# Performance work log

Measured on AMD Instinct MI355X. Metric: run time of the kernel, lower is better.

## Reference

```python
import jax, jax.numpy as jnp
import numpy as np
from jax import lax

H = 512   # hidden_size
O = 256   # output_size
B = 64    # batch
S = 1024  # encoder sequence length
T = 256   # decoder timesteps


def setup_inputs() -> dict:
    key = jax.random.key(0)
    ks = jax.random.split(key, 10)
    bound = 1.0 / np.sqrt(H)  # PyTorch LSTM/Linear init scale
    return {
        "encoder_outputs": jax.random.normal(ks[0], (B, S, H), jnp.float32),
        "hidden": jax.random.normal(ks[1], (1, B, H), jnp.float32),
        "cell": jax.random.normal(ks[2], (1, B, H), jnp.float32),
        "target": jax.random.normal(ks[3], (B, T, O), jnp.float32),
        # LSTM params (gate order i, f, g, o as in PyTorch)
        "W_ih": jax.random.uniform(ks[4], (4 * H, H + O), jnp.float32, -bound, bound),
        "W_hh": jax.random.uniform(ks[5], (4 * H, H), jnp.float32, -bound, bound),
        "b_ih": jax.random.uniform(ks[6], (4 * H,), jnp.float32, -bound, bound),
        "b_hh": jax.random.uniform(ks[7], (4 * H,), jnp.float32, -bound, bound),
        # FC params
        "W_fc": jax.random.uniform(ks[8], (O, H), jnp.float32, -bound, bound),
        "b_fc": jax.random.uniform(ks[9], (O,), jnp.float32, -bound, bound),
    }


def reference(encoder_outputs, hidden, cell, target, W_ih, W_hh, b_ih, b_hh, W_fc, b_fc):
    h0 = hidden[0]  # [B, H]
    c0 = cell[0]    # [B, H]

    def step(carry, x_t):
        h, c = carry
        # Attention: dot-product scores over encoder positions
        scores = jnp.einsum("bsh,bh->bs", encoder_outputs, h)      # [B, S]
        attn = jax.nn.softmax(scores, axis=1)
        context = jnp.einsum("bs,bsh->bh", attn, encoder_outputs)  # [B, H]
        x = jnp.concatenate([context, x_t], axis=-1)               # [B, H+O]
        # Single-step LSTM cell (PyTorch gate order i, f, g, o)
        gates = x @ W_ih.T + b_ih + h @ W_hh.T + b_hh              # [B, 4H]
        i_g, f_g, g_g, o_g = jnp.split(gates, 4, axis=-1)
        i_g = jax.nn.sigmoid(i_g)
        f_g = jax.nn.sigmoid(f_g)
        g_g = jnp.tanh(g_g)
        o_g = jax.nn.sigmoid(o_g)
        c_new = f_g * c + i_g * g_g
        h_new = o_g * jnp.tanh(c_new)
        out = h_new @ W_fc.T + b_fc                                # [B, O]
        return (h_new, c_new), out

    _, outs = lax.scan(step, (h0, c0), jnp.swapaxes(target, 0, 1))  # outs: [T, B, O]
    return jnp.swapaxes(outs, 0, 1)  # [B, T, O]
```

## Files before the change

### kernel.cpp

```cpp
#include <hip/hip_runtime.h>

#define HH 512
#define OO 256
#define BB 64
#define SS 1024
#define TT 256
#define KK 1280

typedef __attribute__((ext_vector_type(8))) short bh8;
typedef __attribute__((ext_vector_type(8))) _Float16 hf8;
typedef __attribute__((ext_vector_type(4))) float fx4;

__device__ __forceinline__ unsigned short f2bf(float x) {
    union { float f; unsigned int u; } v; v.f = x;
    unsigned int r = v.u + 0x7fffu + ((v.u >> 16) & 1u);
    return (unsigned short)(r >> 16);
}
__device__ __forceinline__ float bf2f(unsigned short s) {
    union { unsigned int u; float f; } z; z.u = ((unsigned int)s) << 16; return z.f;
}

__global__ void prep_weights(const float* __restrict__ W_ih,
                             const float* __restrict__ W_hh,
                             unsigned short* __restrict__ wfH,
                             unsigned short* __restrict__ wfL) {
    int g = blockIdx.x * 256 + threadIdx.x;
    if (g >= 64 * 40 * 2 * 64) return;
    int lane = g & 63;
    int nt = (g >> 6) & 1;
    int kk = (g >> 7) % 40;
    int ht = (g >> 7) / 40;
    int c = nt * 16 + (lane & 15);
    int gate = c >> 3, rr = c & 7;
    int j = gate * 512 + ht * 8 + rr;
    int kbase = kk * 32 + (lane >> 4) * 8;
    unsigned short* dh = wfH + (size_t)g * 8;
    unsigned short* dl = wfL + (size_t)g * 8;
#pragma unroll
    for (int r = 0; r < 8; ++r) {
        int k = kbase + r;
        float v = (k < 768) ? W_ih[(size_t)j * 768 + k]
                            : W_hh[(size_t)j * 512 + (k - 768)];
        unsigned short hi = f2bf(v);
        dh[r] = hi;
        dl[r] = f2bf(v - bf2f(hi));
    }
}

__global__ void prep_misc(const float* __restrict__ hidden,
                          const float* __restrict__ cell,
                          float* __restrict__ h, float* __restrict__ c) {
    const int total = 32768 + 32768;
    for (int i = blockIdx.x * 256 + threadIdx.x; i < total; i += gridDim.x * 256) {
        if (i < 32768) h[i] = hidden[i];
        else           c[i - 32768] = cell[i - 32768];
    }
}

__global__ void prep_enc(const float* __restrict__ enc,
                         _Float16* __restrict__ ench) {
    const size_t i = ((size_t)blockIdx.x * 256 + threadIdx.x) * 8;
    const float4 a = *(const float4*)(enc + i);
    const float4 b = *(const float4*)(enc + i + 4);
    hf8 o;
    o[0] = (_Float16)a.x; o[1] = (_Float16)a.y;
    o[2] = (_Float16)a.z; o[3] = (_Float16)a.w;
    o[4] = (_Float16)b.x; o[5] = (_Float16)b.y;
    o[6] = (_Float16)b.z; o[7] = (_Float16)b.w;
    *(hf8*)(ench + i) = o;
}

__device__ __forceinline__ void fc_unit(int v, int tprev,
                                        const float* __restrict__ h,
                                        const float* __restrict__ W_fc,
                                        const float* __restrict__ b_fc,
                                        float* __restrict__ out,
                                        float (*shacc)[64]) {
    const int tid = threadIdx.x;
    const int b = v >> 2, oq = v & 3;
    const int ol = tid & 63, kq = tid >> 6;
    const int o = oq * 64 + ol;
    float acc = 0.f;
    const float* hp = h + b * HH + kq * 128;
    const float* wp = W_fc + (size_t)o * HH + kq * 128;
#pragma unroll 8
    for (int k2 = 0; k2 < 128; ++k2) acc += hp[k2] * wp[k2];
    shacc[kq][ol] = acc;
    __syncthreads();
    if (tid < 64) {
        float vv = shacc[0][tid] + shacc[1][tid]
                 + shacc[2][tid] + shacc[3][tid] + b_fc[oq * 64 + tid];
        out[((size_t)b * TT + tprev) * OO + oq * 64 + tid] = vv;
    }
}

template <int ENCF16>
__global__ void __launch_bounds__(256)
step_attnp(int t, const float* __restrict__ enc,
           const _Float16* __restrict__ ench,
           const float* __restrict__ h,
           float* __restrict__ pm, float* __restrict__ pl,
           float* __restrict__ pctx,
           const float* __restrict__ W_fc, const float* __restrict__ b_fc,
           float* __restrict__ out) {
    const int tid = threadIdx.x;
    const int lane = tid & 63;
    const int w = tid >> 6;

    __shared__ union {
        struct { float m[4]; float l[4]; float ctx[4][512]; } a;
        struct { float acc[4][64]; } o;
    } sh;

    const int u = blockIdx.x;
    if (u < 1024) {
        const int b = u >> 4, ch = u & 15;
        float m = -3.0e38f, l = 0.f;
        if (ENCF16) {
            const float* hb = h + b * HH + lane * 8;
            const float4 h0 = *(const float4*)hb;
            const float4 h1 = *(const float4*)(hb + 4);
            float cx[8];
#pragma unroll
            for (int j = 0; j < 8; ++j) cx[j] = 0.f;
            const _Float16* er =
                ench + ((size_t)(b * SS + ch * 64 + w * 16)) * HH + lane * 8;
            for (int rp = 0; rp < 8; ++rp) {
                const hf8 ev = *(const hf8*)er;
                const hf8 fv = *(const hf8*)(er + HH);
                float e[8], f[8];
#pragma unroll
                for (int j = 0; j < 8; ++j) {
                    e[j] = (float)ev[j];
                    f[j] = (float)fv[j];
                }
                float dA = e[0]*h0.x + e[1]*h0.y + e[2]*h0.z + e[3]*h0.w
                         + e[4]*h1.x + e[5]*h1.y + e[6]*h1.z + e[7]*h1.w;
                float dB = f[0]*h0.x + f[1]*h0.y + f[2]*h0.z + f[3]*h0.w
                         + f[4]*h1.x + f[5]*h1.y + f[6]*h1.z + f[7]*h1.w;
#pragma unroll
                for (int off = 32; off; off >>= 1) {
                    dA += __shfl_xor(dA, off);
                    dB += __shfl_xor(dB, off);
                }
                const float mx = fmaxf(dA, dB);
                if (mx > m) {
                    const float fs = __expf(m - mx);
                    l *= fs;
#pragma unroll
                    for (int j = 0; j < 8; ++j) cx[j] *= fs;
                    m = mx;
                }
                const float pA = __expf(dA - m);
                const float pB = __expf(dB - m);
                l += pA + pB;
#pragma unroll
                for (int j = 0; j < 8; ++j) cx[j] += pA * e[j] + pB * f[j];
                er += 2 * HH;
            }
            if (lane == 0) { sh.a.m[w] = m; sh.a.l[w] = l; }
            *(float4*)&sh.a.ctx[w][lane * 8]     = make_float4(cx[0], cx[1], cx[2], cx[3]);
            *(float4*)&sh.a.ctx[w][lane * 8 + 4] = make_float4(cx[4], cx[5], cx[6], cx[7]);
        } else {
            const float4 h0 = *(const float4*)(h + b * HH + lane * 4);
            const float4 h1 = *(const float4*)(h + b * HH + 256 + lane * 4);
            float4 c0 = {0, 0, 0, 0}, c1 = {0, 0, 0, 0};
            const float* er = enc + ((size_t)(b * SS + ch * 64 + w * 16)) * HH;
            for (int rp = 0; rp < 8; ++rp) {
                const float4 e0 = *(const float4*)(er + lane * 4);
                const float4 e1 = *(const float4*)(er + 256 + lane * 4);
                const float4 f0 = *(const float4*)(er + HH + lane * 4);
                const float4 f1 = *(const float4*)(er + HH + 256 + lane * 4);
                float dA = e0.x * h0.x + e0.y * h0.y + e0.z * h0.z + e0.w * h0.w
                         + e1.x * h1.x + e1.y * h1.y + e1.z * h1.z + e1.w * h1.w;
                float dB = f0.x * h0.x + f0.y * h0.y + f0.z * h0.z + f0.w * h0.w
                         + f1.x * h1.x + f1.y * h1.y + f1.z * h1.z + f1.w * h1.w;
#pragma unroll
                for (int off = 32; off; off >>= 1) {
                    dA += __shfl_xor(dA, off);
                    dB += __shfl_xor(dB, off);
                }
                const float mx = fmaxf(dA, dB);
                if (mx > m) {
                    const float fs = __expf(m - mx);
                    l *= fs;
                    c0.x *= fs; c0.y *= fs; c0.z *= fs; c0.w *= fs;
                    c1.x *= fs; c1.y *= fs; c1.z *= fs; c1.w *= fs;
                    m = mx;
                }
                const float pA = __expf(dA - m);
                const float pB = __expf(dB - m);
                l += pA + pB;
                c0.x += pA * e0.x + pB * f0.x; c0.y += pA * e0.y + pB * f0.y;
                c0.z += pA * e0.z + pB * f0.z; c0.w += pA * e0.w + pB * f0.w;
                c1.x += pA * e1.x + pB * f1.x; c1.y += pA * e1.y + pB * f1.y;
                c1.z += pA * e1.z + pB * f1.z; c1.w += pA * e1.w + pB * f1.w;
                er += 2 * HH;
            }
            if (lane == 0) { sh.a.m[w] = m; sh.a.l[w] = l; }
            *(float4*)&sh.a.ctx[w][lane * 4] = c0;
            *(float4*)&sh.a.ctx[w][256 + lane * 4] = c1;
        }
        __syncthreads();
        float M = fmaxf(fmaxf(sh.a.m[0], sh.a.m[1]), fmaxf(sh.a.m[2], sh.a.m[3]));
        float wg[4]; float ls = 0.f;
#pragma unroll
        for (int q = 0; q < 4; ++q) { wg[q] = __expf(sh.a.m[q] - M); ls += wg[q] * sh.a.l[q]; }
        const int hh = tid * 2;
        float v0 = wg[0] * sh.a.ctx[0][hh] + wg[1] * sh.a.ctx[1][hh]
                 + wg[2] * sh.a.ctx[2][hh] + wg[3] * sh.a.ctx[3][hh];
        float v1 = wg[0] * sh.a.ctx[0][hh + 1] + wg[1] * sh.a.ctx[1][hh + 1]
                 + wg[2] * sh.a.ctx[2][hh + 1] + wg[3] * sh.a.ctx[3][hh + 1];
        float* pc = pctx + ((size_t)(b * 16 + ch)) * HH;
        *(float2*)(pc + hh) = make_float2(v0, v1);
        if (tid == 0) { pm[b * 16 + ch] = M; pl[b * 16 + ch] = ls; }
    } else if (t > 0) {
        fc_unit(u - 1024, t - 1, h, W_fc, b_fc, out, sh.o.acc);
    }
}

__global__ void __launch_bounds__(256)
step_combine(int t, const float* __restrict__ target, const float* __restrict__ h,
             const float* __restrict__ pm, const float* __restrict__ pl,
             const float* __restrict__ pctx,
             unsigned short* __restrict__ xbh, unsigned short* __restrict__ xbl) {
    const int tid = threadIdx.x;
    const int b = blockIdx.x;
    float Mb = -3.0e38f;
#pragma unroll
    for (int q2 = 0; q2 < 16; ++q2) Mb = fmaxf(Mb, pm[b * 16 + q2]);
    float wq[16]; float lsb = 0.f;
#pragma unroll
    for (int q2 = 0; q2 < 16; ++q2) {
        wq[q2] = __expf(pm[b * 16 + q2] - Mb);
        lsb += wq[q2] * pl[b * 16 + q2];
    }
    const float inv = 1.0f / lsb;
    const int h2 = tid * 2;
    float s0 = 0.f, s1 = 0.f;
#pragma unroll
    for (int q2 = 0; q2 < 16; ++q2) {
        const float* pc2 = pctx + ((size_t)(b * 16 + q2)) * HH + h2;
        s0 += wq[q2] * pc2[0];
        s1 += wq[q2] * pc2[1];
    }
    s0 *= inv; s1 *= inv;
    unsigned short a0 = f2bf(s0), a1 = f2bf(s1);
    xbh[b * KK + h2]     = a0;  xbl[b * KK + h2]     = f2bf(s0 - bf2f(a0));
    xbh[b * KK + h2 + 1] = a1;  xbl[b * KK + h2 + 1] = f2bf(s1 - bf2f(a1));
    if (tid < 128) {
        const float* tg = target + ((size_t)b * TT + t) * OO + tid * 2;
        unsigned short t0 = f2bf(tg[0]), t1 = f2bf(tg[1]);
        xbh[b * KK + 512 + tid * 2]     = t0;
        xbh[b * KK + 512 + tid * 2 + 1] = t1;
        xbl[b * KK + 512 + tid * 2]     = f2bf(tg[0] - bf2f(t0));
        xbl[b * KK + 512 + tid * 2 + 1] = f2bf(tg[1] - bf2f(t1));
    }
    const float hv0 = h[b * HH + h2], hv1 = h[b * HH + h2 + 1];
    unsigned short g0 = f2bf(hv0), g1 = f2bf(hv1);
    xbh[b * KK + 768 + h2]     = g0;  xbl[b * KK + 768 + h2]     = f2bf(hv0 - bf2f(g0));
    xbh[b * KK + 768 + h2 + 1] = g1;  xbl[b * KK + 768 + h2 + 1] = f2bf(hv1 - bf2f(g1));
}

__global__ void __launch_bounds__(256)
step_gates(const unsigned short* __restrict__ xbh,
           const unsigned short* __restrict__ xbl,
           const unsigned short* __restrict__ wfH,
           const unsigned short* __restrict__ wfL,
           const float* __restrict__ b_ih, const float* __restrict__ b_hh,
           float* __restrict__ h, float* __restrict__ c) {
    const int tid = threadIdx.x;
    const int lane = tid & 63;
    const int w = tid >> 6;
    __shared__ float g[64][32];

    const int ht = blockIdx.x;
    fx4 a0 = {0, 0, 0, 0}, a1 = {0, 0, 0, 0};
    const int bro = 16 * w + (lane & 15);
    const int kg = lane >> 4;
    const size_t wbase = (size_t)ht * 40 * 2 * 512;
    for (int kk = 0; kk < 40; ++kk) {
        const size_t aoff = (size_t)bro * KK + kk * 32 + kg * 8;
        bh8 avh = *(const bh8*)(xbh + aoff);
        bh8 avl = *(const bh8*)(xbl + aoff);
        bh8 b0h = *(const bh8*)(wfH + wbase + (kk * 2 + 0) * 512 + lane * 8);
        bh8 b1h = *(const bh8*)(wfH + wbase + (kk * 2 + 1) * 512 + lane * 8);
        bh8 b0l = *(const bh8*)(wfL + wbase + (kk * 2 + 0) * 512 + lane * 8);
        bh8 b1l = *(const bh8*)(wfL + wbase + (kk * 2 + 1) * 512 + lane * 8);
        a0 = __builtin_amdgcn_mfma_f32_16x16x32_bf16(avh, b0h, a0, 0, 0, 0);
        a0 = __builtin_amdgcn_mfma_f32_16x16x32_bf16(avl, b0h, a0, 0, 0, 0);
        a0 = __builtin_amdgcn_mfma_f32_16x16x32_bf16(avh, b0l, a0, 0, 0, 0);
        a1 = __builtin_amdgcn_mfma_f32_16x16x32_bf16(avh, b1h, a1, 0, 0, 0);
        a1 = __builtin_amdgcn_mfma_f32_16x16x32_bf16(avl, b1h, a1, 0, 0, 0);
        a1 = __builtin_amdgcn_mfma_f32_16x16x32_bf16(avh, b1l, a1, 0, 0, 0);
    }
    const int crow = (lane >> 4) * 4;
#pragma unroll
    for (int r = 0; r < 4; ++r) {
        g[16 * w + crow + r][lane & 15]        = a0[r];
        g[16 * w + crow + r][16 + (lane & 15)] = a1[r];
    }
    __syncthreads();
#pragma unroll
    for (int p = 0; p < 2; ++p) {
        const int idx = tid * 2 + p;
        const int b = idx >> 3, r = idx & 7;
        const int hidx = ht * 8 + r;
        float gi = g[b][r]      + b_ih[hidx]        + b_hh[hidx];
        float gf = g[b][8 + r]  + b_ih[512 + hidx]  + b_hh[512 + hidx];
        float gg = g[b][16 + r] + b_ih[1024 + hidx] + b_hh[1024 + hidx];
        float go = g[b][24 + r] + b_ih[1536 + hidx] + b_hh[1536 + hidx];
        float ig = 1.f / (1.f + __expf(-gi));
        float fg = 1.f / (1.f + __expf(-gf));
        float g2 = tanhf(gg);
        float og = 1.f / (1.f + __expf(-go));
        float cn = fg * c[b * HH + hidx] + ig * g2;
        float hn = og * tanhf(cn);
        c[b * HH + hidx] = cn;
        h[b * HH + hidx] = hn;
    }
}

__global__ void __launch_bounds__(256)
fc_final(const float* __restrict__ h, const float* __restrict__ W_fc,
         const float* __restrict__ b_fc, float* __restrict__ out) {
    __shared__ float acc[4][64];
    fc_unit(blockIdx.x, TT - 1, h, W_fc, b_fc, out, acc);
}

extern "C" void kernel_launch(void* const* d_in, const int* in_sizes, int n_in,
                              void* d_out, int out_size, void* d_ws, size_t ws_size,
                              hipStream_t stream) {
    const float* enc    = (const float*)d_in[0];
    const float* hidden = (const float*)d_in[1];
    const float* cellp  = (const float*)d_in[2];
    const float* target = (const float*)d_in[3];
    const float* W_ih   = (const float*)d_in[4];
    const float* W_hh   = (const float*)d_in[5];
    const float* b_ih   = (const float*)d_in[6];
    const float* b_hh   = (const float*)d_in[7];
    const float* W_fc   = (const float*)d_in[8];
    const float* b_fc   = (const float*)d_in[9];
    float* out = (float*)d_out;

    char* base = (char*)d_ws;
    float* h              = (float*)(base + 0);
    float* c              = (float*)(base + 131072);
    unsigned short* wfH   = (unsigned short*)(base + 262144);
    unsigned short* wfL   = (unsigned short*)(base + 5505024);
    unsigned short* xbh   = (unsigned short*)(base + 10747904);
    unsigned short* xbl   = (unsigned short*)(base + 10911744);
    float* pm             = (float*)(base + 11075584);
    float* pl             = (float*)(base + 11079680);
    float* pctx           = (float*)(base + 11083776);
    _Float16* ench        = (_Float16*)(base + 13180928);
    const size_t NEED_H = 13180928ULL + 67108864ULL;

    const bool use_ench = (ws_size >= NEED_H);

    prep_weights<<<dim3(1280), dim3(256), 0, stream>>>(W_ih, W_hh, wfH, wfL);
    prep_misc<<<dim3(256), dim3(256), 0, stream>>>(hidden, cellp, h, c);
    if (use_ench)
        prep_enc<<<dim3(16384), dim3(256), 0, stream>>>(enc, ench);

    for (int t = 0; t < TT; ++t) {
        if (use_ench)
            step_attnp<1><<<dim3(1280), dim3(256), 0, stream>>>(
                t, enc, ench, h, pm, pl, pctx, W_fc, b_fc, out);
        else
            step_attnp<0><<<dim3(1280), dim3(256), 0, stream>>>(
                t, enc, ench, h, pm, pl, pctx, W_fc, b_fc, out);
        step_combine<<<dim3(64), dim3(256), 0, stream>>>(
            t, target, h, pm, pl, pctx, xbh, xbl);
        step_gates<<<dim3(64), dim3(256), 0, stream>>>(
            xbh, xbl, wfH, wfL, b_ih, b_hh, h, c);
    }
    fc_final<<<dim3(256), dim3(256), 0, stream>>>(h, W_fc, b_fc, out);
}
```

Before: 10.53 ms.

## Fuse attention partial and combine into one per-batch 1024-thread kernel

Attention now runs one 1024-thread block per batch row (16 waves each covering 64 encoder rows) instead of 16 blocks per batch row. The softmax/context merge and the bf16 hi/lo packing of the LSTM input now happen inside the same kernel, so the separate combine launch and the global partial buffers go away. The FC blocks are also reshaped to one 1024-thread block per batch. This saves a launch and global round-trip per timestep, but drops parallelism from 1280 blocks to 128, which may underuse the GPU's compute units on the bandwidth-heavy attention pass. The fp32 encoder fallback path is removed, so the kernel now always assumes the fp16 workspace is present.

```diff
diff --git a/kernel.cpp b/kernel.cpp
--- a/kernel.cpp
+++ b/kernel.cpp
@@ -70,37 +70,10 @@
     *(hf8*)(ench + i) = o;
 }
 
-__device__ __forceinline__ void fc_unit(int v, int tprev,
-                                        const float* __restrict__ h,
-                                        const float* __restrict__ W_fc,
-                                        const float* __restrict__ b_fc,
-                                        float* __restrict__ out,
-                                        float (*shacc)[64]) {
-    const int tid = threadIdx.x;
-    const int b = v >> 2, oq = v & 3;
-    const int ol = tid & 63, kq = tid >> 6;
-    const int o = oq * 64 + ol;
-    float acc = 0.f;
-    const float* hp = h + b * HH + kq * 128;
-    const float* wp = W_fc + (size_t)o * HH + kq * 128;
-#pragma unroll 8
-    for (int k2 = 0; k2 < 128; ++k2) acc += hp[k2] * wp[k2];
-    shacc[kq][ol] = acc;
-    __syncthreads();
-    if (tid < 64) {
-        float vv = shacc[0][tid] + shacc[1][tid]
-                 + shacc[2][tid] + shacc[3][tid] + b_fc[oq * 64 + tid];
-        out[((size_t)b * TT + tprev) * OO + oq * 64 + tid] = vv;
-    }
-}
-
-template <int ENCF16>
-__global__ void __launch_bounds__(256)
-step_attnp(int t, const float* __restrict__ enc,
-           const _Float16* __restrict__ ench,
-           const float* __restrict__ h,
-           float* __restrict__ pm, float* __restrict__ pl,
-           float* __restrict__ pctx,
+__global__ void __launch_bounds__(1024)
+step_attnx(int t, const _Float16* __restrict__ ench,
+           const float* __restrict__ h, const float* __restrict__ target,
+           unsigned short* __restrict__ xbh, unsigned short* __restrict__ xbl,
            const float* __restrict__ W_fc, const float* __restrict__ b_fc,
            float* __restrict__ out) {
     const int tid = threadIdx.x;
@@ -108,158 +81,107 @@
     const int w = tid >> 6;
 
     __shared__ union {
-        struct { float m[4]; float l[4]; float ctx[4][512]; } a;
-        struct { float acc[4][64]; } o;
+        struct { float m[16]; float l[16]; float ctx[16][512]; } a;
+        struct { float acc[256][4]; } o;
     } sh;
 
-    const int u = blockIdx.x;
-    if (u < 1024) {
-        const int b = u >> 4, ch = u & 15;
+    const int bid = blockIdx.x;
+    if (bid < 64) {
+        const int b = bid;
+        const float* hb = h + b * HH + lane * 8;
+        const float4 h0 = *(const float4*)hb;
+        const float4 h1 = *(const float4*)(hb + 4);
         float m = -3.0e38f, l = 0.f;
-        if (ENCF16) {
-            const float* hb = h + b * HH + lane * 8;
-            const float4 h0 = *(const float4*)hb;
-            const float4 h1 = *(const float4*)(hb + 4);
-            float cx[8];
-#pragma unroll
-            for (int j = 0; j < 8; ++j) cx[j] = 0.f;
-            const _Float16* er =
-                ench + ((size_t)(b * SS + ch * 64 + w * 16)) * HH + lane * 8;
-            for (int rp = 0; rp < 8; ++rp) {
-                const hf8 ev = *(const hf8*)er;
-                const hf8 fv = *(const hf8*)(er + HH);
-                float e[8], f[8];
-#pragma unroll
-                for (int j = 0; j < 8; ++j) {
-                    e[j] = (float)ev[j];
-                    f[j] = (float)fv[j];
-                }
-                float dA = e[0]*h0.x + e[1]*h0.y + e[2]*h0.z + e[3]*h0.w
-                         + e[4]*h1.x + e[5]*h1.y + e[6]*h1.z + e[7]*h1.w;
-                float dB = f[0]*h0.x + f[1]*h0.y + f[2]*h0.z + f[3]*h0.w
-                         + f[4]*h1.x + f[5]*h1.y + f[6]*h1.z + f[7]*h1.w;
-#pragma unroll
-                for (int off = 32; off; off >>= 1) {
-                    dA += __shfl_xor(dA, off);
-                    dB += __shfl_xor(dB, off);
-                }
-                const float mx = fmaxf(dA, dB);
-                if (mx > m) {
-                    const float fs = __expf(m - mx);
-                    l *= fs;
-#pragma unroll
-                    for (int j = 0; j < 8; ++j) cx[j] *= fs;
-                    m = mx;
-                }
-                const float pA = __expf(dA - m);
-                const float pB = __expf(dB - m);
-                l += pA + pB;
-#pragma unroll
-                for (int j = 0; j < 8; ++j) cx[j] += pA * e[j] + pB * f[j];
-                er += 2 * HH;
+        float cx[8];
+#pragma unroll
+        for (int j = 0; j < 8; ++j) cx[j] = 0.f;
+        const _Float16* er = ench + ((size_t)(b * SS + w * 64)) * HH + lane * 8;
+        for (int rp = 0; rp < 32; ++rp) {
+            const hf8 ev = *(const hf8*)er;
+            const hf8 fv = *(const hf8*)(er + HH);
+            float e[8], f[8];
+#pragma unroll
+            for (int j = 0; j < 8; ++j) {
+                e[j] = (float)ev[j];
+                f[j] = (float)fv[j];
             }
-            if (lane == 0) { sh.a.m[w] = m; sh.a.l[w] = l; }
-            *(float4*)&sh.a.ctx[w][lane * 8]     = make_float4(cx[0], cx[1], cx[2], cx[3]);
-            *(float4*)&sh.a.ctx[w][lane * 8 + 4] = make_float4(cx[4], cx[5], cx[6], cx[7]);
+            float dA = e[0]*h0.x + e[1]*h0.y + e[2]*h0.z + e[3]*h0.w
+                     + e[4]*h1.x + e[5]*h1.y + e[6]*h1.z + e[7]*h1.w;
+            float dB = f[0]*h0.x + f[1]*h0.y + f[2]*h0.z + f[3]*h0.w
+                     + f[4]*h1.x + f[5]*h1.y + f[6]*h1.z + f[7]*h1.w;
+#pragma unroll
+            for (int off = 32; off; off >>= 1) {
+                dA += __shfl_xor(dA, off);
+                dB += __shfl_xor(dB, off);
+            }
+            const float mx = fmaxf(dA, dB);
+            if (mx > m) {
+                const float fs = __expf(m - mx);
+                l *= fs;
+#pragma unroll
+                for (int j = 0; j < 8; ++j) cx[j] *= fs;
+                m = mx;
+            }
+            const float pA = __expf(dA - m);
+            const float pB = __expf(dB - m);
+            l += pA + pB;
+#pragma unroll
+            for (int j = 0; j < 8; ++j) cx[j] += pA * e[j] + pB * f[j];
+            er += 2 * HH;
+        }
+        if (lane == 0) { sh.a.m[w] = m; sh.a.l[w] = l; }
+        *(float4*)&sh.a.ctx[w][lane * 8]     = make_float4(cx[0], cx[1], cx[2], cx[3]);
+        *(float4*)&sh.a.ctx[w][lane * 8 + 4] = make_float4(cx[4], cx[5], cx[6], cx[7]);
+        __syncthreads();
+        float M = -3.0e38f;
+#pragma unroll
+        for (int q = 0; q < 16; ++q) M = fmaxf(M, sh.a.m[q]);
+        float wq[16]; float lsb = 0.f;
+#pragma unroll
+        for (int q = 0; q < 16; ++q) {
+            wq[q] = __expf(sh.a.m[q] - M);
+            lsb += wq[q] * sh.a.l[q];
+        }
+        const float inv = 1.0f / lsb;
+        if (tid < 512) {
+            float s = 0.f;
+#pragma unroll
+            for (int q = 0; q < 16; ++q) s += wq[q] * sh.a.ctx[q][tid];
+            s *= inv;
+            const unsigned short a0 = f2bf(s);
+            xbh[b * KK + tid] = a0;
+            xbl[b * KK + tid] = f2bf(s - bf2f(a0));
+        } else if (tid < 768) {
+            const int o = tid - 512;
+            const float tv = target[((size_t)b * TT + t) * OO + o];
+            const unsigned short t0 = f2bf(tv);
+            xbh[b * KK + 512 + o] = t0;
+            xbl[b * KK + 512 + o] = f2bf(tv - bf2f(t0));
         } else {
-            const float4 h0 = *(const float4*)(h + b * HH + lane * 4);
-            const float4 h1 = *(const float4*)(h + b * HH + 256 + lane * 4);
-            float4 c0 = {0, 0, 0, 0}, c1 = {0, 0, 0, 0};
-            const float* er = enc + ((size_t)(b * SS + ch * 64 + w * 16)) * HH;
-            for (int rp = 0; rp < 8; ++rp) {
-                const float4 e0 = *(const float4*)(er + lane * 4);
-                const float4 e1 = *(const float4*)(er + 256 + lane * 4);
-                const float4 f0 = *(const float4*)(er + HH + lane * 4);
-                const float4 f1 = *(const float4*)(er + HH + 256 + lane * 4);
-                float dA = e0.x * h0.x + e0.y * h0.y + e0.z * h0.z + e0.w * h0.w
-                         + e1.x * h1.x + e1.y * h1.y + e1.z * h1.z + e1.w * h1.w;
-                float dB = f0.x * h0.x + f0.y * h0.y + f0.z * h0.z + f0.w * h0.w
-                         + f1.x * h1.x + f1.y * h1.y + f1.z * h1.z + f1.w * h1.w;
-#pragma unroll
-                for (int off = 32; off; off >>= 1) {
-                    dA += __shfl_xor(dA, off);
-                    dB += __shfl_xor(dB, off);
-                }
-                const float mx = fmaxf(dA, dB);
-                if (mx > m) {
-                    const float fs = __expf(m - mx);
-                    l *= fs;
-                    c0.x *= fs; c0.y *= fs; c0.z *= fs; c0.w *= fs;
-                    c1.x *= fs; c1.y *= fs; c1.z *= fs; c1.w *= fs;
-                    m = mx;
-                }
-                const float pA = __expf(dA - m);
-                const float pB = __expf(dB - m);
-                l += pA + pB;
-                c0.x += pA * e0.x + pB * f0.x; c0.y += pA * e0.y + pB * f0.y;
-                c0.z += pA * e0.z + pB * f0.z; c0.w += pA * e0.w + pB * f0.w;
-                c1.x += pA * e1.x + pB * f1.x; c1.y += pA * e1.y + pB * f1.y;
-                c1.z += pA * e1.z + pB * f1.z; c1.w += pA * e1.w + pB * f1.w;
-                er += 2 * HH;
-            }
-            if (lane == 0) { sh.a.m[w] = m; sh.a.l[w] = l; }
-            *(float4*)&sh.a.ctx[w][lane * 4] = c0;
-            *(float4*)&sh.a.ctx[w][256 + lane * 4] = c1;
+            const int h2 = (tid - 768) * 2;
+            const float hv0 = h[b * HH + h2], hv1 = h[b * HH + h2 + 1];
+            const unsigned short g0 = f2bf(hv0), g1 = f2bf(hv1);
+            xbh[b * KK + 768 + h2]     = g0;
+            xbl[b * KK + 768 + h2]     = f2bf(hv0 - bf2f(g0));
+            xbh[b * KK + 768 + h2 + 1] = g1;
+            xbl[b * KK + 768 + h2 + 1] = f2bf(hv1 - bf2f(g1));
         }
+    } else if (t > 0) {
+        const int b = bid - 64;
+        const int o = tid & 255, kq = tid >> 8;
+        float acc = 0.f;
+        const float* hp = h + b * HH + kq * 128;
+        const float* wp = W_fc + (size_t)o * HH + kq * 128;
+#pragma unroll 8
+        for (int k2 = 0; k2 < 128; ++k2) acc += hp[k2] * wp[k2];
+        sh.o.acc[o][kq] = acc;
         __syncthreads();
-        float M = fmaxf(fmaxf(sh.a.m[0], sh.a.m[1]), fmaxf(sh.a.m[2], sh.a.m[3]));
-        float wg[4]; float ls = 0.f;
-#pragma unroll
-        for (int q = 0; q < 4; ++q) { wg[q] = __expf(sh.a.m[q] - M); ls += wg[q] * sh.a.l[q]; }
-        const int hh = tid * 2;
-        float v0 = wg[0] * sh.a.ctx[0][hh] + wg[1] * sh.a.ctx[1][hh]
-                 + wg[2] * sh.a.ctx[2][hh] + wg[3] * sh.a.ctx[3][hh];
-        float v1 = wg[0] * sh.a.ctx[0][hh + 1] + wg[1] * sh.a.ctx[1][hh + 1]
-                 + wg[2] * sh.a.ctx[2][hh + 1] + wg[3] * sh.a.ctx[3][hh + 1];
-        float* pc = pctx + ((size_t)(b * 16 + ch)) * HH;
-        *(float2*)(pc + hh) = make_float2(v0, v1);
-        if (tid == 0) { pm[b * 16 + ch] = M; pl[b * 16 + ch] = ls; }
-    } else if (t > 0) {
-        fc_unit(u - 1024, t - 1, h, W_fc, b_fc, out, sh.o.acc);
-    }
-}
-
-__global__ void __launch_bounds__(256)
-step_combine(int t, const float* __restrict__ target, const float* __restrict__ h,
-             const float* __restrict__ pm, const float* __restrict__ pl,
-             const float* __restrict__ pctx,
-             unsigned short* __restrict__ xbh, unsigned short* __restrict__ xbl) {
-    const int tid = threadIdx.x;
-    const int b = blockIdx.x;
-    float Mb = -3.0e38f;
-#pragma unroll
-    for (int q2 = 0; q2 < 16; ++q2) Mb = fmaxf(Mb, pm[b * 16 + q2]);
-    float wq[16]; float lsb = 0.f;
-#pragma unroll
-    for (int q2 = 0; q2 < 16; ++q2) {
-        wq[q2] = __expf(pm[b * 16 + q2] - Mb);
-        lsb += wq[q2] * pl[b * 16 + q2];
-    }
-    const float inv = 1.0f / lsb;
-    const int h2 = tid * 2;
-    float s0 = 0.f, s1 = 0.f;
-#pragma unroll
-    for (int q2 = 0; q2 < 16; ++q2) {
-        const float* pc2 = pctx + ((size_t)(b * 16 + q2)) * HH + h2;
-        s0 += wq[q2] * pc2[0];
-        s1 += wq[q2] * pc2[1];
-    }
-    s0 *= inv; s1 *= inv;
-    unsigned short a0 = f2bf(s0), a1 = f2bf(s1);
-    xbh[b * KK + h2]     = a0;  xbl[b * KK + h2]     = f2bf(s0 - bf2f(a0));
-    xbh[b * KK + h2 + 1] = a1;  xbl[b * KK + h2 + 1] = f2bf(s1 - bf2f(a1));
-    if (tid < 128) {
-        const float* tg = target + ((size_t)b * TT + t) * OO + tid * 2;
-        unsigned short t0 = f2bf(tg[0]), t1 = f2bf(tg[1]);
-        xbh[b * KK + 512 + tid * 2]     = t0;
-        xbh[b * KK + 512 + tid * 2 + 1] = t1;
-        xbl[b * KK + 512 + tid * 2]     = f2bf(tg[0] - bf2f(t0));
-        xbl[b * KK + 512 + tid * 2 + 1] = f2bf(tg[1] - bf2f(t1));
-    }
-    const float hv0 = h[b * HH + h2], hv1 = h[b * HH + h2 + 1];
-    unsigned short g0 = f2bf(hv0), g1 = f2bf(hv1);
-    xbh[b * KK + 768 + h2]     = g0;  xbl[b * KK + 768 + h2]     = f2bf(hv0 - bf2f(g0));
-    xbh[b * KK + 768 + h2 + 1] = g1;  xbl[b * KK + 768 + h2 + 1] = f2bf(hv1 - bf2f(g1));
+        if (tid < 256) {
+            float vv = sh.o.acc[tid][0] + sh.o.acc[tid][1]
+                     + sh.o.acc[tid][2] + sh.o.acc[tid][3] + b_fc[tid];
+            out[((size_t)b * TT + (t - 1)) * OO + tid] = vv;
+        }
+    }
 }
 
 __global__ void __launch_bounds__(256)
@@ -321,11 +243,24 @@
     }
 }
 
-__global__ void __launch_bounds__(256)
+__global__ void __launch_bounds__(1024)
 fc_final(const float* __restrict__ h, const float* __restrict__ W_fc,
          const float* __restrict__ b_fc, float* __restrict__ out) {
-    __shared__ float acc[4][64];
-    fc_unit(blockIdx.x, TT - 1, h, W_fc, b_fc, out, acc);
+    __shared__ float acc[256][4];
+    const int tid = threadIdx.x;
+    const int b = blockIdx.x;
+    const int o = tid & 255, kq = tid >> 8;
+    float a = 0.f;
+    const float* hp = h + b * HH + kq * 128;
+    const float* wp = W_fc + (size_t)o * HH + kq * 128;
+#pragma unroll 8
+    for (int k2 = 0; k2 < 128; ++k2) a += hp[k2] * wp[k2];
+    acc[o][kq] = a;
+    __syncthreads();
+    if (tid < 256) {
+        float vv = acc[tid][0] + acc[tid][1] + acc[tid][2] + acc[tid][3] + b_fc[tid];
+        out[((size_t)b * TT + (TT - 1)) * OO + tid] = vv;
+    }
 }
 
 extern "C" void kernel_launch(void* const* d_in, const int* in_sizes, int n_in,
@@ -350,30 +285,17 @@
     unsigned short* wfL   = (unsigned short*)(base + 5505024);
     unsigned short* xbh   = (unsigned short*)(base + 10747904);
     unsigned short* xbl   = (unsigned short*)(base + 10911744);
-    float* pm             = (float*)(base + 11075584);
-    float* pl             = (float*)(base + 11079680);
-    float* pctx           = (float*)(base + 11083776);
-    _Float16* ench        = (_Float16*)(base + 13180928);
-    const size_t NEED_H = 13180928ULL + 67108864ULL;
-
-    const bool use_ench = (ws_size >= NEED_H);
+    _Float16* ench        = (_Float16*)(base + 11075584);
 
     prep_weights<<<dim3(1280), dim3(256), 0, stream>>>(W_ih, W_hh, wfH, wfL);
     prep_misc<<<dim3(256), dim3(256), 0, stream>>>(hidden, cellp, h, c);
-    if (use_ench)
-        prep_enc<<<dim3(16384), dim3(256), 0, stream>>>(enc, ench);
+    prep_enc<<<dim3(16384), dim3(256), 0, stream>>>(enc, ench);
 
     for (int t = 0; t < TT; ++t) {
-        if (use_ench)
-            step_attnp<1><<<dim3(1280), dim3(256), 0, stream>>>(
-                t, enc, ench, h, pm, pl, pctx, W_fc, b_fc, out);
-        else
-            step_attnp<0><<<dim3(1280), dim3(256), 0, stream>>>(
-                t, enc, ench, h, pm, pl, pctx, W_fc, b_fc, out);
-        step_combine<<<dim3(64), dim3(256), 0, stream>>>(
-            t, target, h, pm, pl, pctx, xbh, xbl);
+        step_attnx<<<dim3(128), dim3(1024), 0, stream>>>(
+            t, ench, h, target, xbh, xbl, W_fc, b_fc, out);
         step_gates<<<dim3(64), dim3(256), 0, stream>>>(
             xbh, xbl, wfH, wfL, b_ih, b_hh, h, c);
     }
-    fc_final<<<dim3(256), dim3(256), 0, stream>>>(h, W_fc, b_fc, out);
-}
+    fc_final<<<dim3(64), dim3(1024), 0, stream>>>(h, W_fc, b_fc, out);
+}
```

Result: slower. 13.33 ms (+26.6%).

## Compute attention scores with f16 MFMA on a pre-swizzled encoder copy

Applied to the files above, without the earlier changes.

Adds a prep kernel that lays out fp16 encoder data in MFMA fragment order, so attention scores can come from 16x16x32 f16 MFMA against an fp16 copy of h held in shared memory. The per-row shuffle reductions and the online softmax are replaced by a block-wide max/sum followed by a second pass that accumulates the context from a row-major fp16 (or fp32) encoder copy. This moves the score dot products off scalar FMAs, but each step now reads the encoder twice and the workspace needs a second 64MB copy. Rounding h to fp16 may also reduce accuracy.

```diff
diff --git a/kernel.cpp b/kernel.cpp
--- a/kernel.cpp
+++ b/kernel.cpp
@@ -10,20 +10,21 @@
 typedef __attribute__((ext_vector_type(8))) short bh8;
 typedef __attribute__((ext_vector_type(8))) _Float16 hf8;
 typedef __attribute__((ext_vector_type(4))) float fx4;
-
-__device__ __forceinline__ unsigned short f2bf(float x) {
+typedef unsigned short ushort_t;
+
+__device__ __forceinline__ ushort_t f2bf(float x) {
     union { float f; unsigned int u; } v; v.f = x;
     unsigned int r = v.u + 0x7fffu + ((v.u >> 16) & 1u);
-    return (unsigned short)(r >> 16);
-}
-__device__ __forceinline__ float bf2f(unsigned short s) {
+    return (ushort_t)(r >> 16);
+}
+__device__ __forceinline__ float bf2f(ushort_t s) {
     union { unsigned int u; float f; } z; z.u = ((unsigned int)s) << 16; return z.f;
 }
 
 __global__ void prep_weights(const float* __restrict__ W_ih,
                              const float* __restrict__ W_hh,
-                             unsigned short* __restrict__ wfH,
-                             unsigned short* __restrict__ wfL) {
+                             ushort_t* __restrict__ wfH,
+                             ushort_t* __restrict__ wfL) {
     int g = blockIdx.x * 256 + threadIdx.x;
     if (g >= 64 * 40 * 2 * 64) return;
     int lane = g & 63;
@@ -34,14 +35,14 @@
     int gate = c >> 3, rr = c & 7;
     int j = gate * 512 + ht * 8 + rr;
     int kbase = kk * 32 + (lane >> 4) * 8;
-    unsigned short* dh = wfH + (size_t)g * 8;
-    unsigned short* dl = wfL + (size_t)g * 8;
+    ushort_t* dh = wfH + (size_t)g * 8;
+    ushort_t* dl = wfL + (size_t)g * 8;
 #pragma unroll
     for (int r = 0; r < 8; ++r) {
         int k = kbase + r;
         float v = (k < 768) ? W_ih[(size_t)j * 768 + k]
                             : W_hh[(size_t)j * 512 + (k - 768)];
-        unsigned short hi = f2bf(v);
+        ushort_t hi = f2bf(v);
         dh[r] = hi;
         dl[r] = f2bf(v - bf2f(hi));
     }
@@ -57,8 +58,29 @@
     }
 }
 
-__global__ void prep_enc(const float* __restrict__ enc,
-                         _Float16* __restrict__ ench) {
+__global__ void prep_encfrag(const float* __restrict__ enc,
+                             _Float16* __restrict__ encfrag) {
+    const int g = blockIdx.x * 256 + threadIdx.x;
+    const int lane = g & 63;
+    const int kk = (g >> 6) & 15;
+    const int w = (g >> 10) & 3;
+    const int ch = (g >> 12) & 15;
+    const int b = g >> 16;
+    const int s = ch * 64 + w * 16 + (lane & 15);
+    const int k0 = kk * 32 + (lane >> 4) * 8;
+    const float* src = enc + ((size_t)(b * SS + s)) * HH + k0;
+    const float4 a = *(const float4*)src;
+    const float4 bb = *(const float4*)(src + 4);
+    hf8 o;
+    o[0] = (_Float16)a.x;  o[1] = (_Float16)a.y;
+    o[2] = (_Float16)a.z;  o[3] = (_Float16)a.w;
+    o[4] = (_Float16)bb.x; o[5] = (_Float16)bb.y;
+    o[6] = (_Float16)bb.z; o[7] = (_Float16)bb.w;
+    *(hf8*)(encfrag + (size_t)g * 8) = o;
+}
+
+__global__ void prep_ench(const float* __restrict__ enc,
+                          _Float16* __restrict__ ench) {
     const size_t i = ((size_t)blockIdx.x * 256 + threadIdx.x) * 8;
     const float4 a = *(const float4*)(enc + i);
     const float4 b = *(const float4*)(enc + i + 4);
@@ -94,10 +116,10 @@
     }
 }
 
-template <int ENCF16>
+template <int PH2F16>
 __global__ void __launch_bounds__(256)
-step_attnp(int t, const float* __restrict__ enc,
-           const _Float16* __restrict__ ench,
+step_attn6(int t, const _Float16* __restrict__ encfrag,
+           const _Float16* __restrict__ ench, const float* __restrict__ enc32,
            const float* __restrict__ h,
            float* __restrict__ pm, float* __restrict__ pl,
            float* __restrict__ pctx,
@@ -108,112 +130,78 @@
     const int w = tid >> 6;
 
     __shared__ union {
-        struct { float m[4]; float l[4]; float ctx[4][512]; } a;
+        struct { _Float16 h16[512]; float p[64]; float wm[4]; float wl[4]; } a;
         struct { float acc[4][64]; } o;
     } sh;
 
     const int u = blockIdx.x;
     if (u < 1024) {
         const int b = u >> 4, ch = u & 15;
-        float m = -3.0e38f, l = 0.f;
-        if (ENCF16) {
-            const float* hb = h + b * HH + lane * 8;
-            const float4 h0 = *(const float4*)hb;
-            const float4 h1 = *(const float4*)(hb + 4);
-            float cx[8];
-#pragma unroll
-            for (int j = 0; j < 8; ++j) cx[j] = 0.f;
-            const _Float16* er =
-                ench + ((size_t)(b * SS + ch * 64 + w * 16)) * HH + lane * 8;
-            for (int rp = 0; rp < 8; ++rp) {
-                const hf8 ev = *(const hf8*)er;
-                const hf8 fv = *(const hf8*)(er + HH);
-                float e[8], f[8];
-#pragma unroll
-                for (int j = 0; j < 8; ++j) {
-                    e[j] = (float)ev[j];
-                    f[j] = (float)fv[j];
-                }
-                float dA = e[0]*h0.x + e[1]*h0.y + e[2]*h0.z + e[3]*h0.w
-                         + e[4]*h1.x + e[5]*h1.y + e[6]*h1.z + e[7]*h1.w;
-                float dB = f[0]*h0.x + f[1]*h0.y + f[2]*h0.z + f[3]*h0.w
-                         + f[4]*h1.x + f[5]*h1.y + f[6]*h1.z + f[7]*h1.w;
-#pragma unroll
-                for (int off = 32; off; off >>= 1) {
-                    dA += __shfl_xor(dA, off);
-                    dB += __shfl_xor(dB, off);
-                }
-                const float mx = fmaxf(dA, dB);
-                if (mx > m) {
-                    const float fs = __expf(m - mx);
-                    l *= fs;
-#pragma unroll
-                    for (int j = 0; j < 8; ++j) cx[j] *= fs;
-                    m = mx;
-                }
-                const float pA = __expf(dA - m);
-                const float pB = __expf(dB - m);
-                l += pA + pB;
-#pragma unroll
-                for (int j = 0; j < 8; ++j) cx[j] += pA * e[j] + pB * f[j];
-                er += 2 * HH;
+        {
+            const float2 hv = *(const float2*)(h + b * HH + tid * 2);
+            sh.a.h16[tid * 2]     = (_Float16)hv.x;
+            sh.a.h16[tid * 2 + 1] = (_Float16)hv.y;
+        }
+        __syncthreads();
+        const _Float16* af = encfrag + ((size_t)(u * 4 + w) * 16) * 512;
+        fx4 acc = {0.f, 0.f, 0.f, 0.f};
+#pragma unroll
+        for (int kk = 0; kk < 16; ++kk) {
+            const hf8 afr = *(const hf8*)(af + kk * 512 + lane * 8);
+            const hf8 bfr = *(const hf8*)&sh.a.h16[kk * 32 + (lane >> 4) * 8];
+            acc = __builtin_amdgcn_mfma_f32_16x16x32_f16(afr, bfr, acc, 0, 0, 0);
+        }
+        float m4 = fmaxf(fmaxf(acc[0], acc[1]), fmaxf(acc[2], acc[3]));
+        float m16 = fmaxf(m4, __shfl_xor(m4, 16));
+        m16 = fmaxf(m16, __shfl_xor(m16, 32));
+        float e0 = __expf(acc[0] - m16), e1 = __expf(acc[1] - m16);
+        float e2 = __expf(acc[2] - m16), e3 = __expf(acc[3] - m16);
+        float l4 = (e0 + e1) + (e2 + e3);
+        float l16 = l4 + __shfl_xor(l4, 16);
+        l16 += __shfl_xor(l16, 32);
+        if (lane == 0) { sh.a.wm[w] = m16; sh.a.wl[w] = l16; }
+        __syncthreads();
+        const float M = fmaxf(fmaxf(sh.a.wm[0], sh.a.wm[1]),
+                              fmaxf(sh.a.wm[2], sh.a.wm[3]));
+        if ((lane & 15) == 0) {
+            const int rbase = w * 16 + (lane >> 4) * 4;
+            sh.a.p[rbase + 0] = __expf(acc[0] - M);
+            sh.a.p[rbase + 1] = __expf(acc[1] - M);
+            sh.a.p[rbase + 2] = __expf(acc[2] - M);
+            sh.a.p[rbase + 3] = __expf(acc[3] - M);
+        }
+        if (tid == 0) {
+            const float pls = sh.a.wl[0] * __expf(sh.a.wm[0] - M)
+                            + sh.a.wl[1] * __expf(sh.a.wm[1] - M)
+                            + sh.a.wl[2] * __expf(sh.a.wm[2] - M)
+                            + sh.a.wl[3] * __expf(sh.a.wm[3] - M);
+            pm[u] = M;
+            pl[u] = pls;
+        }
+        __syncthreads();
+        const int k0 = tid * 2;
+        float c0 = 0.f, c1 = 0.f;
+        if (PH2F16) {
+            const _Float16* e2p = ench + ((size_t)(b * SS + ch * 64)) * HH + k0;
+            for (int s = 0; s < 64; ++s) {
+                const float ps = sh.a.p[s];
+                c0 += ps * (float)e2p[0];
+                c1 += ps * (float)e2p[1];
+                e2p += HH;
             }
-            if (lane == 0) { sh.a.m[w] = m; sh.a.l[w] = l; }
-            *(float4*)&sh.a.ctx[w][lane * 8]     = make_float4(cx[0], cx[1], cx[2], cx[3]);
-            *(float4*)&sh.a.ctx[w][lane * 8 + 4] = make_float4(cx[4], cx[5], cx[6], cx[7]);
         } else {
-            const float4 h0 = *(const float4*)(h + b * HH + lane * 4);
-            const float4 h1 = *(const float4*)(h + b * HH + 256 + lane * 4);
-            float4 c0 = {0, 0, 0, 0}, c1 = {0, 0, 0, 0};
-            const float* er = enc + ((size_t)(b * SS + ch * 64 + w * 16)) * HH;
-            for (int rp = 0; rp < 8; ++rp) {
-                const float4 e0 = *(const float4*)(er + lane * 4);
-                const float4 e1 = *(const float4*)(er + 256 + lane * 4);
-                const float4 f0 = *(const float4*)(er + HH + lane * 4);
-                const float4 f1 = *(const float4*)(er + HH + 256 + lane * 4);
-                float dA = e0.x * h0.x + e0.y * h0.y + e0.z * h0.z + e0.w * h0.w
-                         + e1.x * h1.x + e1.y * h1.y + e1.z * h1.z + e1.w * h1.w;
-                float dB = f0.x * h0.x + f0.y * h0.y + f0.z * h0.z + f0.w * h0.w
-                         + f1.x * h1.x + f1.y * h1.y + f1.z * h1.z + f1.w * h1.w;
-#pragma unroll
-                for (int off = 32; off; off >>= 1) {
-                    dA += __shfl_xor(dA, off);
-                    dB += __shfl_xor(dB, off);
-                }
-                const float mx = fmaxf(dA, dB);
-                if (mx > m) {
-                    const float fs = __expf(m - mx);
-                    l *= fs;
-                    c0.x *= fs; c0.y *= fs; c0.z *= fs; c0.w *= fs;
-                    c1.x *= fs; c1.y *= fs; c1.z *= fs; c1.w *= fs;
-                    m = mx;
-                }
-                const float pA = __expf(dA - m);
-                const float pB = __expf(dB - m);
-                l += pA + pB;
-                c0.x += pA * e0.x + pB * f0.x; c0.y += pA * e0.y + pB * f0.y;
-                c0.z += pA * e0.z + pB * f0.z; c0.w += pA * e0.w + pB * f0.w;
-                c1.x += pA * e1.x + pB * f1.x; c1.y += pA * e1.y + pB * f1.y;
-                c1.z += pA * e1.z + pB * f1.z; c1.w += pA * e1.w + pB * f1.w;
-                er += 2 * HH;
+            const float* e2p = enc32 + ((size_t)(b * SS + ch * 64)) * HH + k0;
+            for (int s = 0; s < 64; ++s) {
+                const float ps = sh.a.p[s];
+                const float2 ev = *(const float2*)e2p;
+                c0 += ps * ev.x;
+                c1 += ps * ev.y;
+                e2p += HH;
             }
-            if (lane == 0) { sh.a.m[w] = m; sh.a.l[w] = l; }
-            *(float4*)&sh.a.ctx[w][lane * 4] = c0;
-            *(float4*)&sh.a.ctx[w][256 + lane * 4] = c1;
-        }
-        __syncthreads();
-        float M = fmaxf(fmaxf(sh.a.m[0], sh.a.m[1]), fmaxf(sh.a.m[2], sh.a.m[3]));
-        float wg[4]; float ls = 0.f;
-#pragma unroll
-        for (int q = 0; q < 4; ++q) { wg[q] = __expf(sh.a.m[q] - M); ls += wg[q] * sh.a.l[q]; }
-        const int hh = tid * 2;
-        float v0 = wg[0] * sh.a.ctx[0][hh] + wg[1] * sh.a.ctx[1][hh]
-                 + wg[2] * sh.a.ctx[2][hh] + wg[3] * sh.a.ctx[3][hh];
-        float v1 = wg[0] * sh.a.ctx[0][hh + 1] + wg[1] * sh.a.ctx[1][hh + 1]
-                 + wg[2] * sh.a.ctx[2][hh + 1] + wg[3] * sh.a.ctx[3][hh + 1];
-        float* pc = pctx + ((size_t)(b * 16 + ch)) * HH;
-        *(float2*)(pc + hh) = make_float2(v0, v1);
-        if (tid == 0) { pm[b * 16 + ch] = M; pl[b * 16 + ch] = ls; }
+        }
+        float* pc = pctx + (size_t)u * 512 + k0;
+        pc[0] = c0;
+        pc[1] = c1;
     } else if (t > 0) {
         fc_unit(u - 1024, t - 1, h, W_fc, b_fc, out, sh.o.acc);
     }
@@ -223,7 +211,7 @@
 step_combine(int t, const float* __restrict__ target, const float* __restrict__ h,
              const float* __restrict__ pm, const float* __restrict__ pl,
              const float* __restrict__ pctx,
-             unsigned short* __restrict__ xbh, unsigned short* __restrict__ xbl) {
+             ushort_t* __restrict__ xbh, ushort_t* __restrict__ xbl) {
     const int tid = threadIdx.x;
     const int b = blockIdx.x;
     float Mb = -3.0e38f;
@@ -245,28 +233,28 @@
         s1 += wq[q2] * pc2[1];
     }
     s0 *= inv; s1 *= inv;
-    unsigned short a0 = f2bf(s0), a1 = f2bf(s1);
+    ushort_t a0 = f2bf(s0), a1 = f2bf(s1);
     xbh[b * KK + h2]     = a0;  xbl[b * KK + h2]     = f2bf(s0 - bf2f(a0));
     xbh[b * KK + h2 + 1] = a1;  xbl[b * KK + h2 + 1] = f2bf(s1 - bf2f(a1));
     if (tid < 128) {
         const float* tg = target + ((size_t)b * TT + t) * OO + tid * 2;
-        unsigned short t0 = f2bf(tg[0]), t1 = f2bf(tg[1]);
+        ushort_t t0 = f2bf(tg[0]), t1 = f2bf(tg[1]);
         xbh[b * KK + 512 + tid * 2]     = t0;
         xbh[b * KK + 512 + tid * 2 + 1] = t1;
         xbl[b * KK + 512 + tid * 2]     = f2bf(tg[0] - bf2f(t0));
         xbl[b * KK + 512 + tid * 2 + 1] = f2bf(tg[1] - bf2f(t1));
     }
     const float hv0 = h[b * HH + h2], hv1 = h[b * HH + h2 + 1];
-    unsigned short g0 = f2bf(hv0), g1 = f2bf(hv1);
+    ushort_t g0 = f2bf(hv0), g1 = f2bf(hv1);
     xbh[b * KK + 768 + h2]     = g0;  xbl[b * KK + 768 + h2]     = f2bf(hv0 - bf2f(g0));
     xbh[b * KK + 768 + h2 + 1] = g1;  xbl[b * KK + 768 + h2 + 1] = f2bf(hv1 - bf2f(g1));
 }
 
 __global__ void __launch_bounds__(256)
-step_gates(const unsigned short* __restrict__ xbh,
-           const unsigned short* __restrict__ xbl,
-           const unsigned short* __restrict__ wfH,
-           const unsigned short* __restrict__ wfL,
+step_gates(const ushort_t* __restrict__ xbh,
+           const ushort_t* __restrict__ xbl,
+           const ushort_t* __restrict__ wfH,
+           const ushort_t* __restrict__ wfL,
            const float* __restrict__ b_ih, const float* __restrict__ b_hh,
            float* __restrict__ h, float* __restrict__ c) {
     const int tid = threadIdx.x;
@@ -344,32 +332,34 @@
     float* out = (float*)d_out;
 
     char* base = (char*)d_ws;
-    float* h              = (float*)(base + 0);
-    float* c              = (float*)(base + 131072);
-    unsigned short* wfH   = (unsigned short*)(base + 262144);
-    unsigned short* wfL   = (unsigned short*)(base + 5505024);
-    unsigned short* xbh   = (unsigned short*)(base + 10747904);
-    unsigned short* xbl   = (unsigned short*)(base + 10911744);
-    float* pm             = (float*)(base + 11075584);
-    float* pl             = (float*)(base + 11079680);
-    float* pctx           = (float*)(base + 11083776);
-    _Float16* ench        = (_Float16*)(base + 13180928);
-    const size_t NEED_H = 13180928ULL + 67108864ULL;
-
-    const bool use_ench = (ws_size >= NEED_H);
+    float* h            = (float*)(base + 0);
+    float* c            = (float*)(base + 131072);
+    ushort_t* wfH       = (ushort_t*)(base + 262144);
+    ushort_t* wfL       = (ushort_t*)(base + 5505024);
+    ushort_t* xbh       = (ushort_t*)(base + 10747904);
+    ushort_t* xbl       = (ushort_t*)(base + 10911744);
+    float* pm           = (float*)(base + 11075584);
+    float* pl           = (float*)(base + 11079680);
+    float* pctx         = (float*)(base + 11083776);
+    _Float16* encfrag   = (_Float16*)(base + 13180928);
+    _Float16* ench      = (_Float16*)(base + 80289792);
+    const size_t NEED_PH2 = 80289792ULL + 67108864ULL;
+
+    const bool f16p2 = (ws_size >= NEED_PH2);
 
     prep_weights<<<dim3(1280), dim3(256), 0, stream>>>(W_ih, W_hh, wfH, wfL);
     prep_misc<<<dim3(256), dim3(256), 0, stream>>>(hidden, cellp, h, c);
-    if (use_ench)
-        prep_enc<<<dim3(16384), dim3(256), 0, stream>>>(enc, ench);
+    prep_encfrag<<<dim3(16384), dim3(256), 0, stream>>>(enc, encfrag);
+    if (f16p2)
+        prep_ench<<<dim3(16384), dim3(256), 0, stream>>>(enc, ench);
 
     for (int t = 0; t < TT; ++t) {
-        if (use_ench)
-            step_attnp<1><<<dim3(1280), dim3(256), 0, stream>>>(
-                t, enc, ench, h, pm, pl, pctx, W_fc, b_fc, out);
+        if (f16p2)
+            step_attn6<1><<<dim3(1280), dim3(256), 0, stream>>>(
+                t, encfrag, ench, enc, h, pm, pl, pctx, W_fc, b_fc, out);
         else
-            step_attnp<0><<<dim3(1280), dim3(256), 0, stream>>>(
-                t, enc, ench, h, pm, pl, pctx, W_fc, b_fc, out);
+            step_attn6<0><<<dim3(1280), dim3(256), 0, stream>>>(
+                t, encfrag, ench, enc, h, pm, pl, pctx, W_fc, b_fc, out);
         step_combine<<<dim3(64), dim3(256), 0, stream>>>(
             t, target, h, pm, pl, pctx, xbh, xbl);
         step_gates<<<dim3(64), dim3(256), 0, stream>>>(
```

Result: slower. 12.97 ms (+23.3%).
